# Kernel tuning notes

Hardware: AMD Instinct MI355X
Metric: run time of the kernel (lower is better)

Reference implementation:

```python
import jax, jax.numpy as jnp
import numpy as np

DIM = 1024
NUM_HEADS = 16
HEAD_DIM = DIM // NUM_HEADS


def _rope(x):
    # x: (B*H, L, hd). ESM-style rotary embedding with rotate_half.
    L, hd = x.shape[1], x.shape[2]
    inv_freq = 1.0 / (10000.0 ** (jnp.arange(0, hd, 2, dtype=jnp.float32) / hd))
    t = jnp.arange(L, dtype=jnp.float32)
    freqs = t[:, None] * inv_freq[None, :]          # (L, hd/2)
    emb = jnp.concatenate([freqs, freqs], axis=-1)   # (L, hd)
    cos, sin = jnp.cos(emb), jnp.sin(emb)
    x1, x2 = jnp.split(x, 2, axis=-1)
    rot = jnp.concatenate([-x2, x1], axis=-1)
    return x * cos + rot * sin


def setup_inputs() -> dict:
    key = jax.random.key(0)
    ks = jax.random.split(key, 10)
    L, N, D = 2048, 1, DIM
    query = jax.random.normal(ks[0], (L, N, D), dtype=jnp.float32)
    asym_ids = jnp.sort(jax.random.randint(ks[1], (N, L), 0, 4), axis=-1)
    s = 0.02
    wq = s * jax.random.normal(ks[2], (D, D), dtype=jnp.float32)
    wk = s * jax.random.normal(ks[3], (D, D), dtype=jnp.float32)
    wv = s * jax.random.normal(ks[4], (D, D), dtype=jnp.float32)
    wo = s * jax.random.normal(ks[5], (D, D), dtype=jnp.float32)
    bq = s * jax.random.normal(ks[6], (D,), dtype=jnp.float32)
    bk = s * jax.random.normal(ks[7], (D,), dtype=jnp.float32)
    bv = s * jax.random.normal(ks[8], (D,), dtype=jnp.float32)
    bo = s * jax.random.normal(ks[9], (D,), dtype=jnp.float32)
    return {"query": query, "asym_ids": asym_ids, "wq": wq, "bq": bq,
            "wk": wk, "bk": bk, "wv": wv, "bv": bv, "wo": wo, "bo": bo}


def reference(query, asym_ids, wq, bq, wk, bk, wv, bv, wo, bo):
    L, N, D = query.shape
    H, hd = NUM_HEADS, HEAD_DIM
    scaling = 1.0 / np.sqrt(hd)

    q = (query @ wq.T + bq) * scaling
    k = query @ wk.T + bk
    v = query @ wv.T + bv

    def to_bh(x):  # (L, N, D) -> (N*H, L, hd)
        return x.reshape(L, N * H, hd).transpose(1, 0, 2)

    q, k, v = to_bh(q), to_bh(k), to_bh(v)

    # raw scores (pre-RoPE), rpe scores (post-RoPE)
    raw = jnp.einsum('ble,bme->blm', q, k).reshape(N, H, L, L)
    qr, kr = _rope(q), _rope(k)
    rpe = jnp.einsum('ble,bme->blm', qr, kr).reshape(N, H, L, L)

    avg = jnp.mean(rpe - raw, axis=(0, 1), keepdims=True)          # (1,1,L,L)
    asym_mask = asym_ids[:, :, None] == asym_ids[:, None, :]        # (N,L,L)
    attn_weights = jnp.where(asym_mask[:, None], rpe, raw + avg)    # (N,H,L,L)

    probs = jax.nn.softmax(attn_weights, axis=-1)
    attn = jnp.einsum('nhlm,nhme->nhle', probs, v.reshape(N, H, L, hd))
    attn = attn.transpose(2, 0, 1, 3).reshape(L, N, D)
    out = attn @ wo.T + bo
    attn_weights_avg = jnp.mean(probs, axis=1)  # (N, L, L)
    return out, attn_weights_avg
```

## Files before the change

kernel.cpp:

```cpp
#include <hip/hip_runtime.h>

#define L 2048
#define D 1024
#define NH 16
#define HD 64
#define SPLIT 4
#define JCH (L / SPLIT)
#define LOG2E 1.4426950408889634f

typedef __attribute__((ext_vector_type(8))) short bf16x8;
typedef __attribute__((ext_vector_type(4))) float f32x4;

#define MFMA(a, b, c) __builtin_amdgcn_mfma_f32_16x16x32_bf16(a, b, c, 0, 0, 0)

__device__ __forceinline__ short f2bf(float x) {
  unsigned u = __float_as_uint(x);
  u = (u + 0x7FFFu + ((u >> 16) & 1u)) >> 16;
  return (short)u;
}

__device__ __forceinline__ void gll16(const void* g, void* l) {
  __builtin_amdgcn_global_load_lds(
      (const __attribute__((address_space(1))) void*)(uintptr_t)g,
      (__attribute__((address_space(3))) void*)(unsigned)(uintptr_t)l, 16, 0, 0);
}

__global__ void trig_kernel(float* __restrict__ costab, float* __restrict__ sintab) {
  int idx = blockIdx.x * blockDim.x + threadIdx.x;
  int t = idx >> 5, fi = idx & 31;
  float f = exp2f(-(float)fi * (13.287712379549449f / 32.0f));
  float ang = (float)t * f;
  costab[idx] = cosf(ang);
  sintab[idx] = sinf(ang);
}

__global__ void f2bf_all_kernel(const float* __restrict__ q,
                                const float* __restrict__ w0, const float* __restrict__ w1,
                                const float* __restrict__ w2, const float* __restrict__ w3,
                                short* __restrict__ dq, short* __restrict__ d0,
                                short* __restrict__ d1, short* __restrict__ d2,
                                short* __restrict__ d3) {
  int i = blockIdx.x * 256 + threadIdx.x;
  const float* src;
  short* dst;
  int off;
  if (i < L * D / 4) {
    src = q; dst = dq; off = i;
  } else {
    int j = i - L * D / 4;
    int seg = j >> 18;
    off = j & (262144 - 1);
    src = seg == 0 ? w0 : seg == 1 ? w1 : seg == 2 ? w2 : w3;
    dst = seg == 0 ? d0 : seg == 1 ? d1 : seg == 2 ? d2 : d3;
  }
  float4 v = ((const float4*)src)[off];
  short4 o;
  o.x = f2bf(v.x); o.y = f2bf(v.y); o.z = f2bf(v.z); o.w = f2bf(v.w);
  ((short4*)dst)[off] = o;
}

__global__ __launch_bounds__(256) void proj3_kernel(
    const short* __restrict__ X,
    const short* __restrict__ Wq, const short* __restrict__ Wk, const short* __restrict__ Wv,
    const float* __restrict__ bq, const float* __restrict__ bk, const float* __restrict__ bv,
    const float* __restrict__ costab, const float* __restrict__ sintab,
    short* __restrict__ Qs, short* __restrict__ QRb, short* __restrict__ Kbb,
    short* __restrict__ KRb, short* __restrict__ Vt) {
  int mode = blockIdx.z;
  const short* W = mode == 0 ? Wq : (mode == 1 ? Wk : Wv);
  const float* bias = mode == 0 ? bq : (mode == 1 ? bk : bv);
  short* out_main = mode == 0 ? Qs : (mode == 1 ? Kbb : Vt);
  short* out_rope = mode == 0 ? QRb : KRb;

  int w = threadIdx.x >> 6, lane = threadIdx.x & 63;
  int c = lane & 15, g = lane >> 4;
  int wi0 = blockIdx.y * 128 + (w >> 1) * 64;
  int wj0 = blockIdx.x * 128 + (w & 1) * 64;

  f32x4 acc[4][4];
#pragma unroll
  for (int m = 0; m < 4; ++m)
#pragma unroll
    for (int n = 0; n < 4; ++n) acc[m][n] = (f32x4){0.f, 0.f, 0.f, 0.f};

  for (int k0 = 0; k0 < D; k0 += 32) {
    bf16x8 aF[4], bF[4];
#pragma unroll
    for (int m = 0; m < 4; ++m)
      aF[m] = *(const bf16x8*)(X + (size_t)(wi0 + m * 16 + c) * D + k0 + g * 8);
#pragma unroll
    for (int n = 0; n < 4; ++n)
      bF[n] = *(const bf16x8*)(W + (size_t)(wj0 + n * 16 + c) * D + k0 + g * 8);
#pragma unroll
    for (int m = 0; m < 4; ++m)
#pragma unroll
      for (int n = 0; n < 4; ++n) acc[m][n] = MFMA(aF[m], bF[n], acc[m][n]);
  }

  float scale = (mode == 0) ? 0.125f * LOG2E : 1.0f;
#pragma unroll
  for (int m = 0; m < 4; ++m) {
#pragma unroll
    for (int r = 0; r < 4; ++r) {
      int i = wi0 + m * 16 + g * 4 + r;
      float v4[4];
#pragma unroll
      for (int n = 0; n < 4; ++n)
        v4[n] = (acc[m][n][r] + bias[wj0 + n * 16 + c]) * scale;
      if (mode == 2) {
#pragma unroll
        for (int n = 0; n < 4; ++n) {
          int col = wj0 + n * 16 + c;
          out_main[(size_t)col * L + i] = f2bf(v4[n]);
        }
      } else {
#pragma unroll
        for (int n = 0; n < 4; ++n) {
          int col = wj0 + n * 16 + c;
          out_main[(size_t)i * D + col] = f2bf(v4[n]);
          float rot = (n < 2) ? -v4[n + 2] : v4[n - 2];
          int fidx = i * 32 + (n & 1) * 16 + c;
          float vr = v4[n] * costab[fidx] + rot * sintab[fidx];
          out_rope[(size_t)i * D + col] = f2bf(vr);
        }
      }
    }
  }
}

__global__ __launch_bounds__(256) void avg_kernel(
    const short* __restrict__ QR, const short* __restrict__ KR,
    const short* __restrict__ Qs, const short* __restrict__ Kb,
    f32x4* __restrict__ avg4) {
  int w = threadIdx.x >> 6, lane = threadIdx.x & 63;
  int c = lane & 15, g = lane >> 4;
  int wi0 = blockIdx.y * 128 + (w >> 1) * 64;
  int wj0 = blockIdx.x * 64 + (w & 1) * 32;

  f32x4 acc1[4][2], acc2[4][2];
#pragma unroll
  for (int m = 0; m < 4; ++m)
#pragma unroll
    for (int n = 0; n < 2; ++n) {
      acc1[m][n] = (f32x4){0.f, 0.f, 0.f, 0.f};
      acc2[m][n] = (f32x4){0.f, 0.f, 0.f, 0.f};
    }

  for (int k0 = 0; k0 < D; k0 += 32) {
    bf16x8 aF[4], a2F[4], bF[2], b2F[2];
#pragma unroll
    for (int m = 0; m < 4; ++m) {
      aF[m] = *(const bf16x8*)(QR + (size_t)(wi0 + m * 16 + c) * D + k0 + g * 8);
      a2F[m] = *(const bf16x8*)(Qs + (size_t)(wi0 + m * 16 + c) * D + k0 + g * 8);
    }
#pragma unroll
    for (int n = 0; n < 2; ++n) {
      bF[n] = *(const bf16x8*)(KR + (size_t)(wj0 + n * 16 + c) * D + k0 + g * 8);
      b2F[n] = *(const bf16x8*)(Kb + (size_t)(wj0 + n * 16 + c) * D + k0 + g * 8);
    }
#pragma unroll
    for (int m = 0; m < 4; ++m)
#pragma unroll
      for (int n = 0; n < 2; ++n) {
        acc1[m][n] = MFMA(aF[m], bF[n], acc1[m][n]);
        acc2[m][n] = MFMA(a2F[m], b2F[n], acc2[m][n]);
      }
  }

#pragma unroll
  for (int m = 0; m < 4; ++m)
#pragma unroll
    for (int n = 0; n < 2; ++n) {
      int j = wj0 + n * 16 + c;
      f32x4 o;
#pragma unroll
      for (int r = 0; r < 4; ++r) o[r] = (acc1[m][n][r] - acc2[m][n][r]) * 0.0625f;
      avg4[(size_t)(((wi0 + m * 16) >> 2) + g) * L + j] = o;
    }
}

__global__ __launch_bounds__(256) void flash3_kernel(
    const short* __restrict__ Qs, const short* __restrict__ Kb,
    const short* __restrict__ QR, const short* __restrict__ KR,
    const short* __restrict__ Vt, const f32x4* __restrict__ avg4,
    const int* __restrict__ ids, float* __restrict__ m_part,
    float* __restrict__ l_part, float* __restrict__ acc_part) {
  int h = blockIdx.y, sp = blockIdx.z;
  int w = threadIdx.x >> 6, lane = threadIdx.x & 63;
  int c = lane & 15, g = lane >> 4;
  int i0 = blockIdx.x * 64 + w * 16;
  int hk = h * 64;

  __shared__ short kb_lds[2][64 * 64];
  __shared__ short kr_lds[2][64 * 64];
  __shared__ short plds[4][16][64];

  int srow = lane >> 3;
  int sxor = (lane & 7) ^ srow;
  int r0a = w * 16, r0b = w * 16 + 8;

  bf16x8 qA[2], qrA[2];
  {
    const short* qp = Qs + (size_t)(i0 + c) * D + hk + g * 8;
    const short* qrp = QR + (size_t)(i0 + c) * D + hk + g * 8;
    qA[0] = *(const bf16x8*)qp;   qA[1] = *(const bf16x8*)(qp + 32);
    qrA[0] = *(const bf16x8*)qrp; qrA[1] = *(const bf16x8*)(qrp + 32);
  }

  int idi[4];
  float mrun[4], lsum[4];
  f32x4 acc[4];
#pragma unroll
  for (int r = 0; r < 4; ++r) {
    idi[r] = ids[i0 + g * 4 + r];
    mrun[r] = -3.0e38f;
    lsum[r] = 0.f;
  }
#pragma unroll
  for (int n = 0; n < 4; ++n) acc[n] = (f32x4){0.f, 0.f, 0.f, 0.f};

  int ifirst = __shfl(idi[0], 0);
  bool iu = __all((idi[0] == idi[1]) & (idi[1] == idi[2]) & (idi[2] == idi[3]) &
                  (idi[0] == ifirst));

  const f32x4* avrow = avg4 + (size_t)((i0 >> 2) + g) * L;
  int jbase = sp * JCH;
  const int NT = JCH / 64;

  gll16(Kb + (size_t)(jbase + r0a + srow) * D + hk + sxor * 8, &kb_lds[0][r0a * 64]);
  gll16(Kb + (size_t)(jbase + r0b + srow) * D + hk + sxor * 8, &kb_lds[0][r0b * 64]);
  gll16(KR + (size_t)(jbase + r0a + srow) * D + hk + sxor * 8, &kr_lds[0][r0a * 64]);
  gll16(KR + (size_t)(jbase + r0b + srow) * D + hk + sxor * 8, &kr_lds[0][r0b * 64]);

  f32x4 avn[4];
  int idjn[4];
#pragma unroll
  for (int sub = 0; sub < 4; ++sub) {
    avn[sub] = avrow[jbase + sub * 16 + c];
    idjn[sub] = ids[jbase + sub * 16 + c];
  }
  __syncthreads();

  int cur = 0;
  for (int jt = 0; jt < NT; ++jt) {
    int jb = jbase + jt * 64;

    if (jt + 1 < NT) {
      int jn = jb + 64;
      short* kd = &kb_lds[cur ^ 1][0];
      short* rd = &kr_lds[cur ^ 1][0];
      gll16(Kb + (size_t)(jn + r0a + srow) * D + hk + sxor * 8, kd + r0a * 64);
      gll16(Kb + (size_t)(jn + r0b + srow) * D + hk + sxor * 8, kd + r0b * 64);
      gll16(KR + (size_t)(jn + r0a + srow) * D + hk + sxor * 8, rd + r0a * 64);
      gll16(KR + (size_t)(jn + r0b + srow) * D + hk + sxor * 8, rd + r0b * 64);
    }

    bf16x8 vf0[4], vf1[4];
#pragma unroll
    for (int n = 0; n < 4; ++n) {
      const short* vp = Vt + (size_t)(hk + n * 16 + c) * L + jb + g * 8;
      vf0[n] = *(const bf16x8*)vp;
      vf1[n] = *(const bf16x8*)(vp + 32);
    }

    f32x4 av[4];
    int idj[4];
#pragma unroll
    for (int sub = 0; sub < 4; ++sub) { av[sub] = avn[sub]; idj[sub] = idjn[sub]; }
    if (jt + 1 < NT) {
#pragma unroll
      for (int sub = 0; sub < 4; ++sub) {
        avn[sub] = avrow[jb + 64 + sub * 16 + c];
        idjn[sub] = ids[jb + 64 + sub * 16 + c];
      }
    }

    int jfirst = __shfl(idj[0], 0);
    bool ju = __all((idj[0] == idj[1]) & (idj[1] == idj[2]) & (idj[2] == idj[3]) &
                    (idj[0] == jfirst));

    const short* kbb = &kb_lds[cur][c * 64];
    const short* krb = &kr_lds[cur][c * 64];
    int co0 = (g ^ (c & 7)) * 8;
    int co1 = ((4 + g) ^ (c & 7)) * 8;

    float t[4][4];
    if (iu && ju && ifirst == jfirst) {
#pragma unroll
      for (int sub = 0; sub < 4; ++sub) {
        bf16x8 kr0 = *(const bf16x8*)(krb + sub * 1024 + co0);
        bf16x8 kr1 = *(const bf16x8*)(krb + sub * 1024 + co1);
        f32x4 z = (f32x4){0.f, 0.f, 0.f, 0.f};
        f32x4 rp = MFMA(qrA[1], kr1, MFMA(qrA[0], kr0, z));
#pragma unroll
        for (int r = 0; r < 4; ++r) t[sub][r] = rp[r];
      }
    } else if (iu && ju) {
#pragma unroll
      for (int sub = 0; sub < 4; ++sub) {
        bf16x8 k0 = *(const bf16x8*)(kbb + sub * 1024 + co0);
        bf16x8 k1 = *(const bf16x8*)(kbb + sub * 1024 + co1);
        f32x4 z = (f32x4){0.f, 0.f, 0.f, 0.f};
        f32x4 rw = MFMA(qA[1], k1, MFMA(qA[0], k0, z));
#pragma unroll
        for (int r = 0; r < 4; ++r) t[sub][r] = rw[r] + av[sub][r];
      }
    } else {
#pragma unroll
      for (int sub = 0; sub < 4; ++sub) {
        bf16x8 k0 = *(const bf16x8*)(kbb + sub * 1024 + co0);
        bf16x8 k1 = *(const bf16x8*)(kbb + sub * 1024 + co1);
        bf16x8 kr0 = *(const bf16x8*)(krb + sub * 1024 + co0);
        bf16x8 kr1 = *(const bf16x8*)(krb + sub * 1024 + co1);
        f32x4 z = (f32x4){0.f, 0.f, 0.f, 0.f};
        f32x4 rw = MFMA(qA[1], k1, MFMA(qA[0], k0, z));
        f32x4 rp = MFMA(qrA[1], kr1, MFMA(qrA[0], kr0, z));
#pragma unroll
        for (int r = 0; r < 4; ++r)
          t[sub][r] = (idi[r] == idj[sub]) ? rp[r] : (rw[r] + av[sub][r]);
      }
    }

    float tm[4];
#pragma unroll
    for (int r = 0; r < 4; ++r)
      tm[r] = fmaxf(fmaxf(t[0][r], t[1][r]), fmaxf(t[2][r], t[3][r]));
    bool ok = (tm[0] <= mrun[0] + 8.f) && (tm[1] <= mrun[1] + 8.f) &&
              (tm[2] <= mrun[2] + 8.f) && (tm[3] <= mrun[3] + 8.f);
    if (!__all(ok)) {
#pragma unroll
      for (int r = 0; r < 4; ++r) {
        float m2 = tm[r];
#pragma unroll
        for (int d = 1; d < 16; d <<= 1) m2 = fmaxf(m2, __shfl_xor(m2, d));
        float mn = fmaxf(mrun[r], m2);
        float so = exp2f(mrun[r] - mn);
        mrun[r] = mn;
        lsum[r] *= so;
#pragma unroll
        for (int n = 0; n < 4; ++n) acc[n][r] *= so;
      }
    }

#pragma unroll
    for (int sub = 0; sub < 4; ++sub)
#pragma unroll
      for (int r = 0; r < 4; ++r) {
        float p = exp2f(t[sub][r] - mrun[r]);
        lsum[r] += p;
        int prow = g * 4 + r;
        plds[w][prow][(sub * 16 + c) ^ ((prow & 7) << 3)] = f2bf(p);
      }

    {
      int pc0 = (g * 8) ^ ((c & 7) << 3);
      int pc1 = (32 + g * 8) ^ ((c & 7) << 3);
      bf16x8 pa = *(const bf16x8*)(&plds[w][c][pc0]);
#pragma unroll
      for (int n = 0; n < 4; ++n) acc[n] = MFMA(pa, vf0[n], acc[n]);
      bf16x8 pb = *(const bf16x8*)(&plds[w][c][pc1]);
#pragma unroll
      for (int n = 0; n < 4; ++n) acc[n] = MFMA(pb, vf1[n], acc[n]);
    }

    __syncthreads();
    cur ^= 1;
  }

#pragma unroll
  for (int r = 0; r < 4; ++r) {
#pragma unroll
    for (int d = 1; d < 16; d <<= 1) lsum[r] += __shfl_xor(lsum[r], d);
  }
  size_t sb = (size_t)(sp * NH + h) * L;
  if (c == 0) {
#pragma unroll
    for (int r = 0; r < 4; ++r) {
      m_part[sb + i0 + g * 4 + r] = mrun[r];
      l_part[sb + i0 + g * 4 + r] = lsum[r];
    }
  }
#pragma unroll
  for (int n = 0; n < 4; ++n)
#pragma unroll
    for (int r = 0; r < 4; ++r)
      acc_part[(sb + i0 + g * 4 + r) * HD + n * 16 + c] = acc[n][r];
}

__global__ void merge_kernel(const float* __restrict__ m_part,
                             const float* __restrict__ l_part,
                             const float* __restrict__ acc_part,
                             float* __restrict__ mfin, float* __restrict__ lfin,
                             short* __restrict__ attn_bf) {
  int idx = blockIdx.x * 256 + threadIdx.x;
  int d = idx & (HD - 1);
  int hi = idx >> 6;
  int i = hi & (L - 1), h = hi >> 11;
  float m4 = -3.0e38f;
#pragma unroll
  for (int s = 0; s < SPLIT; ++s)
    m4 = fmaxf(m4, m_part[(size_t)(s * NH + h) * L + i]);
  float l = 0.f, o = 0.f;
#pragma unroll
  for (int s = 0; s < SPLIT; ++s) {
    size_t sb = (size_t)(s * NH + h) * L + i;
    float e = exp2f(m_part[sb] - m4);
    l += l_part[sb] * e;
    o += acc_part[sb * HD + d] * e;
  }
  attn_bf[(size_t)i * D + h * HD + d] = f2bf(o / l);
  if (d == 0) { mfin[h * L + i] = m4; lfin[h * L + i] = l; }
}

__global__ __launch_bounds__(256) void pavg_kernel(
    const short* __restrict__ Qs, const short* __restrict__ Kb,
    const short* __restrict__ QR, const short* __restrict__ KR,
    const f32x4* __restrict__ avg4, const int* __restrict__ ids,
    const float* __restrict__ m_ws, const float* __restrict__ l_ws,
    float* __restrict__ out1) {
  int j0 = blockIdx.x * 64;
  int iblk = blockIdx.y * 64;
  int w = threadIdx.x >> 6, lane = threadIdx.x & 63;
  int c = lane & 15, g = lane >> 4;
  int i0 = iblk + w * 16;

  __shared__ short kb_lds[2][64 * 64];
  __shared__ short kr_lds[2][64 * 64];
  __shared__ float mS[NH][64], lS[NH][64];

  int srow = lane >> 3;
  int sxor = (lane & 7) ^ srow;
  int r0a = w * 16, r0b = w * 16 + 8;

  int si0 = ids[iblk], si1 = ids[iblk + 63];
  int sj0 = ids[j0], sj1 = ids[j0 + 63];
  int mode = (si0 == si1 && sj0 == sj1) ? ((si0 == sj0) ? 0 : 1) : 2;

  for (int idx = threadIdx.x; idx < NH * 64; idx += 256) {
    int hh = idx >> 6, rr = idx & 63;
    mS[hh][rr] = m_ws[hh * L + iblk + rr];
    lS[hh][rr] = 1.0f / l_ws[hh * L + iblk + rr];
  }

  if (mode != 0) {
    gll16(Kb + (size_t)(j0 + r0a + srow) * D + sxor * 8, &kb_lds[0][r0a * 64]);
    gll16(Kb + (size_t)(j0 + r0b + srow) * D + sxor * 8, &kb_lds[0][r0b * 64]);
  }
  if (mode != 1) {
    gll16(KR + (size_t)(j0 + r0a + srow) * D + sxor * 8, &kr_lds[0][r0a * 64]);
    gll16(KR + (size_t)(j0 + r0b + srow) * D + sxor * 8, &kr_lds[0][r0b * 64]);
  }

  int idi[4], idj[4];
  f32x4 av[4];
  {
    const f32x4* avrow = avg4 + (size_t)((i0 >> 2) + g) * L;
#pragma unroll
    for (int sub = 0; sub < 4; ++sub) {
      av[sub] = avrow[j0 + sub * 16 + c];
      idj[sub] = ids[j0 + sub * 16 + c];
    }
#pragma unroll
    for (int r = 0; r < 4; ++r) idi[r] = ids[i0 + g * 4 + r];
  }

  f32x4 psum[4];
#pragma unroll
  for (int sub = 0; sub < 4; ++sub) psum[sub] = (f32x4){0.f, 0.f, 0.f, 0.f};

  const short* qbase = Qs + (size_t)(i0 + c) * D + g * 8;
  const short* qrbase = QR + (size_t)(i0 + c) * D + g * 8;

  bf16x8 nq0, nq1, nqr0, nqr1;
  if (mode != 0) { nq0 = *(const bf16x8*)qbase; nq1 = *(const bf16x8*)(qbase + 32); }
  if (mode != 1) { nqr0 = *(const bf16x8*)qrbase; nqr1 = *(const bf16x8*)(qrbase + 32); }

  __syncthreads();

  int cur = 0;
#pragma unroll 1
  for (int hh = 0; hh < NH; ++hh) {
    if (hh + 1 < NH) {
      int hkn = (hh + 1) * 64;
      short* kd = &kb_lds[cur ^ 1][0];
      short* rd = &kr_lds[cur ^ 1][0];
      if (mode != 0) {
        gll16(Kb + (size_t)(j0 + r0a + srow) * D + hkn + sxor * 8, kd + r0a * 64);
        gll16(Kb + (size_t)(j0 + r0b + srow) * D + hkn + sxor * 8, kd + r0b * 64);
      }
      if (mode != 1) {
        gll16(KR + (size_t)(j0 + r0a + srow) * D + hkn + sxor * 8, rd + r0a * 64);
        gll16(KR + (size_t)(j0 + r0b + srow) * D + hkn + sxor * 8, rd + r0b * 64);
      }
    }

    bf16x8 q0 = nq0, q1 = nq1, qr0 = nqr0, qr1 = nqr1;
    if (hh + 1 < NH) {
      int hkn = (hh + 1) * 64;
      if (mode != 0) {
        nq0 = *(const bf16x8*)(qbase + hkn);
        nq1 = *(const bf16x8*)(qbase + hkn + 32);
      }
      if (mode != 1) {
        nqr0 = *(const bf16x8*)(qrbase + hkn);
        nqr1 = *(const bf16x8*)(qrbase + hkn + 32);
      }
    }

    const short* kbb = &kb_lds[cur][c * 64];
    const short* krb = &kr_lds[cur][c * 64];
    int co0 = (g ^ (c & 7)) * 8;
    int co1 = ((4 + g) ^ (c & 7)) * 8;

    f32x4 m4 = *(const f32x4*)(&mS[hh][w * 16 + g * 4]);
    f32x4 l4 = *(const f32x4*)(&lS[hh][w * 16 + g * 4]);

    if (mode == 0) {
#pragma unroll
      for (int sub = 0; sub < 4; ++sub) {
        bf16x8 kr0 = *(const bf16x8*)(krb + sub * 1024 + co0);
        bf16x8 kr1 = *(const bf16x8*)(krb + sub * 1024 + co1);
        f32x4 z = (f32x4){0.f, 0.f, 0.f, 0.f};
        f32x4 rp = MFMA(qr1, kr1, MFMA(qr0, kr0, z));
#pragma unroll
        for (int r = 0; r < 4; ++r)
          psum[sub][r] += exp2f(rp[r] - m4[r]) * l4[r];
      }
    } else if (mode == 1) {
#pragma unroll
      for (int sub = 0; sub < 4; ++sub) {
        bf16x8 k0 = *(const bf16x8*)(kbb + sub * 1024 + co0);
        bf16x8 k1 = *(const bf16x8*)(kbb + sub * 1024 + co1);
        f32x4 z = (f32x4){0.f, 0.f, 0.f, 0.f};
        f32x4 rw = MFMA(q1, k1, MFMA(q0, k0, z));
#pragma unroll
        for (int r = 0; r < 4; ++r)
          psum[sub][r] += exp2f(rw[r] + av[sub][r] - m4[r]) * l4[r];
      }
    } else {
#pragma unroll
      for (int sub = 0; sub < 4; ++sub) {
        bf16x8 k0 = *(const bf16x8*)(kbb + sub * 1024 + co0);
        bf16x8 k1 = *(const bf16x8*)(kbb + sub * 1024 + co1);
        bf16x8 kr0 = *(const bf16x8*)(krb + sub * 1024 + co0);
        bf16x8 kr1 = *(const bf16x8*)(krb + sub * 1024 + co1);
        f32x4 z = (f32x4){0.f, 0.f, 0.f, 0.f};
        f32x4 rw = MFMA(q1, k1, MFMA(q0, k0, z));
        f32x4 rp = MFMA(qr1, kr1, MFMA(qr0, kr0, z));
#pragma unroll
        for (int r = 0; r < 4; ++r) {
          float s = (idi[r] == idj[sub]) ? rp[r] : (rw[r] + av[sub][r]);
          psum[sub][r] += exp2f(s - m4[r]) * l4[r];
        }
      }
    }

    __syncthreads();
    cur ^= 1;
  }

#pragma unroll
  for (int sub = 0; sub < 4; ++sub)
#pragma unroll
    for (int r = 0; r < 4; ++r)
      out1[(size_t)(i0 + g * 4 + r) * L + j0 + sub * 16 + c] = psum[sub][r] * 0.0625f;
}

__global__ __launch_bounds__(256) void outproj_kernel(
    const short* __restrict__ A, const short* __restrict__ W,
    const float* __restrict__ bias, float* __restrict__ out) {
  int w = threadIdx.x >> 6, lane = threadIdx.x & 63;
  int c = lane & 15, g = lane >> 4;
  int wi0 = blockIdx.y * 64 + (w >> 1) * 32;
  int wj0 = blockIdx.x * 64 + (w & 1) * 32;

  f32x4 acc[2][2];
#pragma unroll
  for (int m = 0; m < 2; ++m)
#pragma unroll
    for (int n = 0; n < 2; ++n) acc[m][n] = (f32x4){0.f, 0.f, 0.f, 0.f};

  for (int k0 = 0; k0 < D; k0 += 32) {
    bf16x8 aF[2], bF[2];
#pragma unroll
    for (int m = 0; m < 2; ++m)
      aF[m] = *(const bf16x8*)(A + (size_t)(wi0 + m * 16 + c) * D + k0 + g * 8);
#pragma unroll
    for (int n = 0; n < 2; ++n)
      bF[n] = *(const bf16x8*)(W + (size_t)(wj0 + n * 16 + c) * D + k0 + g * 8);
#pragma unroll
    for (int m = 0; m < 2; ++m)
#pragma unroll
      for (int n = 0; n < 2; ++n) acc[m][n] = MFMA(aF[m], bF[n], acc[m][n]);
  }

#pragma unroll
  for (int m = 0; m < 2; ++m)
#pragma unroll
    for (int n = 0; n < 2; ++n)
#pragma unroll
      for (int r = 0; r < 4; ++r) {
        int i = wi0 + m * 16 + g * 4 + r;
        int col = wj0 + n * 16 + c;
        out[(size_t)i * D + col] = acc[m][n][r] + bias[col];
      }
}

extern "C" void kernel_launch(void* const* d_in, const int* in_sizes, int n_in,
                              void* d_out, int out_size, void* d_ws, size_t ws_size,
                              hipStream_t stream) {
  const float* query = (const float*)d_in[0];
  const int* ids = (const int*)d_in[1];
  const float* wq = (const float*)d_in[2];
  const float* bq = (const float*)d_in[3];
  const float* wk = (const float*)d_in[4];
  const float* bk = (const float*)d_in[5];
  const float* wv = (const float*)d_in[6];
  const float* bv = (const float*)d_in[7];
  const float* wo = (const float*)d_in[8];
  const float* bo = (const float*)d_in[9];

  char* p = (char*)d_ws;
  auto carve = [&](size_t bytes) {
    char* r = p;
    p += (bytes + 255) & ~(size_t)255;
    return r;
  };
  short* Xbf = (short*)carve((size_t)L * D * 2);
  short* Wqb = (short*)carve((size_t)D * D * 2);
  short* Wkb = (short*)carve((size_t)D * D * 2);
  short* Wvb = (short*)carve((size_t)D * D * 2);
  short* Wob = (short*)carve((size_t)D * D * 2);
  short* Qs = (short*)carve((size_t)L * D * 2);
  short* QRb = (short*)carve((size_t)L * D * 2);
  short* Kbb = (short*)carve((size_t)L * D * 2);
  short* KRb = (short*)carve((size_t)L * D * 2);
  short* Vt = (short*)carve((size_t)L * D * 2);
  f32x4* avg4 = (f32x4*)carve((size_t)L * L * 4);
  float* m_ws = (float*)carve((size_t)NH * L * 4);
  float* l_ws = (float*)carve((size_t)NH * L * 4);
  short* attn_bf = (short*)carve((size_t)L * D * 2);
  float* costab = (float*)carve((size_t)L * 32 * 4);
  float* sintab = (float*)carve((size_t)L * 32 * 4);
  float* m_part = (float*)carve((size_t)SPLIT * NH * L * 4);
  float* l_part = (float*)carve((size_t)SPLIT * NH * L * 4);
  float* acc_part = (float*)carve((size_t)SPLIT * NH * L * HD * 4);

  float* out0 = (float*)d_out;
  float* out1 = out0 + (size_t)L * D;

  trig_kernel<<<(L * 32) / 256, 256, 0, stream>>>(costab, sintab);

  f2bf_all_kernel<<<(L * D / 4 + 4 * (D * D / 4)) / 256, 256, 0, stream>>>(
      query, wq, wk, wv, wo, Xbf, Wqb, Wkb, Wvb, Wob);

  proj3_kernel<<<dim3(D / 128, L / 128, 3), 256, 0, stream>>>(
      Xbf, Wqb, Wkb, Wvb, bq, bk, bv, costab, sintab, Qs, QRb, Kbb, KRb, Vt);

  avg_kernel<<<dim3(L / 64, L / 128), 256, 0, stream>>>(QRb, KRb, Qs, Kbb, avg4);

  flash3_kernel<<<dim3(L / 64, NH, SPLIT), 256, 0, stream>>>(
      Qs, Kbb, QRb, KRb, Vt, avg4, ids, m_part, l_part, acc_part);

  merge_kernel<<<(NH * L * HD) / 256, 256, 0, stream>>>(m_part, l_part, acc_part,
                                                        m_ws, l_ws, attn_bf);

  pavg_kernel<<<dim3(L / 64, L / 64), 256, 0, stream>>>(Qs, Kbb, QRb, KRb, avg4, ids,
                                                        m_ws, l_ws, out1);

  outproj_kernel<<<dim3(D / 64, L / 64), 256, 0, stream>>>(attn_bf, Wob, bo, out0);
}
```

Measured before the change: 351.9 us.

## Skip avg tiles fully inside same-asym blocks, merge prep kernels

The avg kernel now exits early for tiles where every row and column shares one asym id, because those entries select the rpe score and never read avg. The trig-table and bf16-conversion kernels are merged into one launch, and the hand-written bf16 rounding is replaced with the HIP intrinsic. The skip relies on asym_ids being sorted, so checking the endpoints of each tile is enough, and consumers must never read avg for masked-in entries.

```diff
diff --git a/kernel.cpp b/kernel.cpp
--- a/kernel.cpp
+++ b/kernel.cpp
@@ -1,4 +1,5 @@
 #include <hip/hip_runtime.h>
+#include <hip/hip_bf16.h>
 
 #define L 2048
 #define D 1024
@@ -14,9 +15,8 @@
 #define MFMA(a, b, c) __builtin_amdgcn_mfma_f32_16x16x32_bf16(a, b, c, 0, 0, 0)
 
 __device__ __forceinline__ short f2bf(float x) {
-  unsigned u = __float_as_uint(x);
-  u = (u + 0x7FFFu + ((u >> 16) & 1u)) >> 16;
-  return (short)u;
+  __hip_bfloat16 h = __float2bfloat16(x);
+  return *reinterpret_cast<short*>(&h);
 }
 
 __device__ __forceinline__ void gll16(const void* g, void* l) {
@@ -25,29 +25,30 @@
       (__attribute__((address_space(3))) void*)(unsigned)(uintptr_t)l, 16, 0, 0);
 }
 
-__global__ void trig_kernel(float* __restrict__ costab, float* __restrict__ sintab) {
-  int idx = blockIdx.x * blockDim.x + threadIdx.x;
-  int t = idx >> 5, fi = idx & 31;
-  float f = exp2f(-(float)fi * (13.287712379549449f / 32.0f));
-  float ang = (float)t * f;
-  costab[idx] = cosf(ang);
-  sintab[idx] = sinf(ang);
-}
-
-__global__ void f2bf_all_kernel(const float* __restrict__ q,
-                                const float* __restrict__ w0, const float* __restrict__ w1,
-                                const float* __restrict__ w2, const float* __restrict__ w3,
-                                short* __restrict__ dq, short* __restrict__ d0,
-                                short* __restrict__ d1, short* __restrict__ d2,
-                                short* __restrict__ d3) {
+__global__ void prep_kernel(const float* __restrict__ q,
+                            const float* __restrict__ w0, const float* __restrict__ w1,
+                            const float* __restrict__ w2, const float* __restrict__ w3,
+                            float* __restrict__ costab, float* __restrict__ sintab,
+                            short* __restrict__ dq, short* __restrict__ d0,
+                            short* __restrict__ d1, short* __restrict__ d2,
+                            short* __restrict__ d3) {
   int i = blockIdx.x * 256 + threadIdx.x;
+  if (i < 65536) {
+    int t = i >> 5, fi = i & 31;
+    float f = exp2f(-(float)fi * (13.287712379549449f / 32.0f));
+    float ang = (float)t * f;
+    costab[i] = cosf(ang);
+    sintab[i] = sinf(ang);
+    return;
+  }
+  int i2 = i - 65536;
   const float* src;
   short* dst;
   int off;
-  if (i < L * D / 4) {
-    src = q; dst = dq; off = i;
+  if (i2 < L * D / 4) {
+    src = q; dst = dq; off = i2;
   } else {
-    int j = i - L * D / 4;
+    int j = i2 - L * D / 4;
     int seg = j >> 18;
     off = j & (262144 - 1);
     src = seg == 0 ? w0 : seg == 1 ? w1 : seg == 2 ? w2 : w3;
@@ -131,11 +132,15 @@
 __global__ __launch_bounds__(256) void avg_kernel(
     const short* __restrict__ QR, const short* __restrict__ KR,
     const short* __restrict__ Qs, const short* __restrict__ Kb,
-    f32x4* __restrict__ avg4) {
+    const int* __restrict__ ids, f32x4* __restrict__ avg4) {
+  int ib = blockIdx.y * 128, jb = blockIdx.x * 64;
+  if (ids[ib] == ids[ib + 127] && ids[jb] == ids[jb + 63] && ids[ib] == ids[jb])
+    return;
+
   int w = threadIdx.x >> 6, lane = threadIdx.x & 63;
   int c = lane & 15, g = lane >> 4;
-  int wi0 = blockIdx.y * 128 + (w >> 1) * 64;
-  int wj0 = blockIdx.x * 64 + (w & 1) * 32;
+  int wi0 = ib + (w >> 1) * 64;
+  int wj0 = jb + (w & 1) * 32;
 
   f32x4 acc1[4][2], acc2[4][2];
 #pragma unroll
@@ -649,15 +654,13 @@
   float* out0 = (float*)d_out;
   float* out1 = out0 + (size_t)L * D;
 
-  trig_kernel<<<(L * 32) / 256, 256, 0, stream>>>(costab, sintab);
-
-  f2bf_all_kernel<<<(L * D / 4 + 4 * (D * D / 4)) / 256, 256, 0, stream>>>(
-      query, wq, wk, wv, wo, Xbf, Wqb, Wkb, Wvb, Wob);
+  prep_kernel<<<(65536 + L * D / 4 + 4 * (D * D / 4)) / 256, 256, 0, stream>>>(
+      query, wq, wk, wv, wo, costab, sintab, Xbf, Wqb, Wkb, Wvb, Wob);
 
   proj3_kernel<<<dim3(D / 128, L / 128, 3), 256, 0, stream>>>(
       Xbf, Wqb, Wkb, Wvb, bq, bk, bv, costab, sintab, Qs, QRb, Kbb, KRb, Vt);
 
-  avg_kernel<<<dim3(L / 64, L / 128), 256, 0, stream>>>(QRb, KRb, Qs, Kbb, avg4);
+  avg_kernel<<<dim3(L / 64, L / 128), 256, 0, stream>>>(QRb, KRb, Qs, Kbb, ids, avg4);
 
   flash3_kernel<<<dim3(L / 64, NH, SPLIT), 256, 0, stream>>>(
       Qs, Kbb, QRb, KRb, Vt, avg4, ids, m_part, l_part, acc_part);
```

After: 347.6 us, median of 2. About the same (-1.2%).
